# Kernel tuning notes

Measured on AMD Instinct MI355X. Metric: run time of the kernel, lower is better.

The kernel has to match this reference:

```python
import jax, jax.numpy as jnp
import numpy as np

M = 10000; D = 10000; FG = 256; FD = 256; K = 64
EX = 320000; EY = 320000


def setup_inputs() -> dict:
    key = jax.random.key(0)
    ks = jax.random.split(key, 32)
    s = 0.05  # weight scale
    inp = {}
    inp['x_m'] = jax.random.normal(ks[0], (M, FG), jnp.float32)
    inp['x_d'] = jax.random.normal(ks[1], (D, FD), jnp.float32)
    inp['edge_index_x'] = jax.random.randint(ks[2], (2, EX), 0, M)
    inp['edge_index_y'] = jax.random.randint(ks[3], (2, EY), 0, D)
    # GAT layer params (PyG layout: W [in, H*C], att [H, C], bias [H*C])
    inp['Wx1'] = jax.random.normal(ks[4], (FG, 2 * FG), jnp.float32) * s
    inp['ax1_src'] = jax.random.normal(ks[5], (2, FG), jnp.float32) * s
    inp['ax1_dst'] = jax.random.normal(ks[6], (2, FG), jnp.float32) * s
    inp['bx1'] = jnp.zeros((2 * FG,), jnp.float32)
    inp['Wx2'] = jax.random.normal(ks[7], (2 * FG, FG), jnp.float32) * s
    inp['ax2_src'] = jax.random.normal(ks[8], (1, FG), jnp.float32) * s
    inp['ax2_dst'] = jax.random.normal(ks[9], (1, FG), jnp.float32) * s
    inp['bx2'] = jnp.zeros((FG,), jnp.float32)
    inp['Wy1'] = jax.random.normal(ks[10], (FD, 2 * FD), jnp.float32) * s
    inp['ay1_src'] = jax.random.normal(ks[11], (2, FD), jnp.float32) * s
    inp['ay1_dst'] = jax.random.normal(ks[12], (2, FD), jnp.float32) * s
    inp['by1'] = jnp.zeros((2 * FD,), jnp.float32)
    inp['Wy2'] = jax.random.normal(ks[13], (2 * FD, FD), jnp.float32) * s
    inp['ay2_src'] = jax.random.normal(ks[14], (1, FD), jnp.float32) * s
    inp['ay2_dst'] = jax.random.normal(ks[15], (1, FD), jnp.float32) * s
    inp['by2'] = jnp.zeros((FD,), jnp.float32)
    # MLP heads
    inp['lwx1'] = jax.random.normal(ks[16], (FG, 256), jnp.float32) * s
    inp['lbx1'] = jnp.zeros((256,), jnp.float32)
    inp['lwx2'] = jax.random.normal(ks[17], (256, 128), jnp.float32) * s
    inp['lbx2'] = jnp.zeros((128,), jnp.float32)
    inp['lwx3'] = jax.random.normal(ks[18], (128, K), jnp.float32) * s
    inp['lbx3'] = jnp.zeros((K,), jnp.float32)
    inp['lwy1'] = jax.random.normal(ks[19], (FD, 256), jnp.float32) * s
    inp['lby1'] = jnp.zeros((256,), jnp.float32)
    inp['lwy2'] = jax.random.normal(ks[20], (256, 128), jnp.float32) * s
    inp['lby2'] = jnp.zeros((128,), jnp.float32)
    inp['lwy3'] = jax.random.normal(ks[21], (128, K), jnp.float32) * s
    inp['lby3'] = jnp.zeros((K,), jnp.float32)
    return inp


def gat_conv(x, src, dst, W, a_src, a_dst, b, n):
    # PyG GATConv, add_self_loops=False, negative_slope=0.2, concat=True
    H, C = a_src.shape
    xp = (x @ W).reshape(-1, H, C)                      # [N, H, C]
    al_s = jnp.einsum('nhc,hc->nh', xp, a_src)          # [N, H]
    al_d = jnp.einsum('nhc,hc->nh', xp, a_dst)
    e = jax.nn.leaky_relu(al_s[src] + al_d[dst], 0.2)   # [E, H]
    # softmax over edges grouped by destination node
    mx = jax.ops.segment_max(e, dst, num_segments=n)
    ee = jnp.exp(e - mx[dst])
    denom = jax.ops.segment_sum(ee, dst, num_segments=n)
    alpha = ee / (denom[dst] + 1e-16)                   # [E, H]
    out = jax.ops.segment_sum(xp[src] * alpha[:, :, None], dst, num_segments=n)
    return out.reshape(n, H * C) + b


def mlp3(h, w1, b1, w2, b2, w3, b3):
    h = jax.nn.relu(h @ w1 + b1)
    h = jax.nn.relu(h @ w2 + b2)
    return jax.nn.relu(h @ w3 + b3)


def reference(x_m, x_d, edge_index_x, edge_index_y,
              Wx1, ax1_src, ax1_dst, bx1, Wx2, ax2_src, ax2_dst, bx2,
              Wy1, ay1_src, ay1_dst, by1, Wy2, ay2_src, ay2_dst, by2,
              lwx1, lbx1, lwx2, lbx2, lwx3, lbx3,
              lwy1, lby1, lwy2, lby2, lwy3, lby3):
    sx, dx = edge_index_x[0], edge_index_x[1]
    sy, dy = edge_index_y[0], edge_index_y[1]
    X1 = jax.nn.relu(gat_conv(x_m, sx, dx, Wx1, ax1_src, ax1_dst, bx1, M))
    X = jax.nn.relu(gat_conv(X1, sx, dx, Wx2, ax2_src, ax2_dst, bx2, M))
    Y1 = jax.nn.relu(gat_conv(x_d, sy, dy, Wy1, ay1_src, ay1_dst, by1, D))
    Y = jax.nn.relu(gat_conv(Y1, sy, dy, Wy2, ay2_src, ay2_dst, by2, D))
    x = mlp3(X, lwx1, lbx1, lwx2, lbx2, lwx3, lbx3)     # [M, K]
    y = mlp3(Y, lwy1, lby1, lwy2, lby2, lwy3, lby3)     # [D, K]
    return x @ y.T                                      # [M, D]
```

## Files before the change

kernel.cpp:

```cpp
#include <hip/hip_runtime.h>
#include <cstddef>
#include <cstdint>

#define NODES 10000
#define EDGES 320000

typedef __attribute__((ext_vector_type(8))) short bf16x8;
typedef __attribute__((ext_vector_type(4))) float f32x4;

__device__ inline short bf16rn(float x){
    union { float f; unsigned u; } v; v.f = x;
    unsigned r = (v.u + 0x7FFFu + ((v.u >> 16) & 1u)) >> 16;
    return (short)r;
}
__device__ inline float bf16tof(short h){
    union { float f; unsigned u; } v; v.u = ((unsigned)(unsigned short)h) << 16;
    return v.f;
}

__global__ void count2_kernel(const int* __restrict__ ex, const int* __restrict__ ey,
                              int* __restrict__ counts){
    int e = blockIdx.x*256 + threadIdx.x;
    if (e < 2*EDGES){
        int d = (e < EDGES) ? ex[EDGES + e] : (ey[e] + NODES);
        atomicAdd(&counts[d], 1);
    }
}

__global__ __launch_bounds__(1024) void scan_kernel(const int* __restrict__ counts,
                                                    int* __restrict__ rowptr, int N){
    __shared__ int part[1024];
    int t = threadIdx.x;
    int chunk = (N + 1023) / 1024;
    int b0 = t * chunk;
    int s = 0;
    for (int i=0;i<chunk;i++){ int idx=b0+i; if (idx<N) s += counts[idx]; }
    part[t] = s;
    __syncthreads();
    for (int off=1; off<1024; off<<=1){
        int v = (t>=off) ? part[t-off] : 0;
        __syncthreads();
        part[t] += v;
        __syncthreads();
    }
    int excl = (t==0) ? 0 : part[t-1];
    for (int i=0;i<chunk;i++){
        int idx=b0+i;
        if (idx<N){ rowptr[idx]=excl; excl += counts[idx]; }
    }
    if (t==1023) rowptr[N] = part[1023];
}

__global__ void fill2_kernel(const int* __restrict__ ex, const int* __restrict__ ey,
                             int* __restrict__ cursor, int* __restrict__ col){
    int e = blockIdx.x*256 + threadIdx.x;
    if (e < 2*EDGES){
        int s, d;
        if (e < EDGES){ s = ex[e]; d = ex[EDGES+e]; }
        else          { s = ey[e-EDGES] + NODES; d = ey[e] + NODES; }
        int p = atomicAdd(&cursor[d], 1);
        col[p] = s;
    }
}

struct WtJob { const float* W; const float* a; float* out; int K; int H; int h; };
struct WtJobs { WtJob j[12]; };
__global__ __launch_bounds__(256) void wtilde_kernel(WtJobs js){
    WtJob jb = js.j[blockIdx.x];
    const int C = 256;
    for (int k = threadIdx.x; k < jb.K; k += 256){
        const float* wr = jb.W + (size_t)k*(jb.H*C) + jb.h*C;
        const float* ar = jb.a + jb.h*C;
        float s = 0.f;
        for (int c=0;c<C;c++) s += wr[c]*ar[c];
        jb.out[k*jb.H + jb.h] = s;
    }
}

struct StJob { const float* B; short* th; short* tl; int K; int N; };
struct StJobs { StJob j[10]; };
__global__ __launch_bounds__(256) void splitT_batch(StJobs js){
    StJob jb = js.j[blockIdx.z];
    int n0 = blockIdx.x*32, k0 = blockIdx.y*32;
    if (n0 >= jb.N || k0 >= jb.K) return;
    __shared__ float tile[32][33];
    int tx = threadIdx.x, ty = threadIdx.y;
    #pragma unroll
    for (int r=0;r<4;r++){ int k = ty + r*8; tile[k][tx] = jb.B[(size_t)(k0+k)*jb.N + n0 + tx]; }
    __syncthreads();
    #pragma unroll
    for (int r=0;r<4;r++){
        int n = ty + r*8;
        float v = tile[tx][n];
        short h = bf16rn(v);
        jb.th[(size_t)(n0+n)*jb.K + k0 + tx] = h;
        jb.tl[(size_t)(n0+n)*jb.K + k0 + tx] = bf16rn(v - bf16tof(h));
    }
}

__global__ void split_in_kernel(const float* __restrict__ x0, const float* __restrict__ x1,
                                short* __restrict__ h, short* __restrict__ l){
    int i = (blockIdx.x*256 + threadIdx.x)*4;
    const int HALF = NODES*256;
    if (i >= 2*HALF) return;
    const float* src = (i < HALF) ? (x0 + i) : (x1 + (i - HALF));
    float4 v = *(const float4*)src;
    short h0=bf16rn(v.x), h1=bf16rn(v.y), h2=bf16rn(v.z), h3=bf16rn(v.w);
    short4 hv; hv.x=h0; hv.y=h1; hv.z=h2; hv.w=h3;
    short4 lv; lv.x=bf16rn(v.x-bf16tof(h0)); lv.y=bf16rn(v.y-bf16tof(h1));
    lv.z=bf16rn(v.z-bf16tof(h2)); lv.w=bf16rn(v.w-bf16tof(h3));
    *(short4*)&h[i] = hv;
    *(short4*)&l[i] = lv;
}

struct GemmJob {
    const short* Ah; const short* Al; const short* Bh; const short* Bl;
    float* C; short* Ch; short* Cl; const float* bias;
};
__global__ __launch_bounds__(256) void gemm_ps(GemmJob j0, GemmJob j1,
        int Mr, int Nr, int Kr, int relu)
{
    GemmJob j = (blockIdx.z == 0) ? j0 : j1;
    __shared__ short Ash[96][88], Asl[96][88], Bsh[64][88], Bsl[64][88];
    int t = threadIdx.x;
    int lane = t & 63, wave = t >> 6;
    int wm = (wave >> 1) * 48, wn = (wave & 1) * 32;
    int m0 = blockIdx.y * 96, n0 = blockIdx.x * 64;

    f32x4 acc[3][2];
    #pragma unroll
    for (int i=0;i<3;i++)
      #pragma unroll
      for (int jj=0;jj<2;jj++)
        #pragma unroll
        for (int r=0;r<4;r++) acc[i][jj][r] = 0.f;

    int arow = t >> 3;
    int ablk = (t & 7) * 8;

    for (int k0 = 0; k0 < Kr; k0 += 64){
        #pragma unroll
        for (int rep=0; rep<3; rep++){
            int row = arow + rep*32;
            int gr = m0 + row; gr = gr < Mr ? gr : Mr-1;
            size_t off = (size_t)gr*Kr + k0 + ablk;
            *(int4*)&Ash[row][ablk] = *(const int4*)&j.Ah[off];
            *(int4*)&Asl[row][ablk] = *(const int4*)&j.Al[off];
        }
        #pragma unroll
        for (int rep=0; rep<2; rep++){
            int row = arow + rep*32;
            int gn = n0 + row; gn = gn < Nr ? gn : Nr-1;
            size_t off = (size_t)gn*Kr + k0 + ablk;
            *(int4*)&Bsh[row][ablk] = *(const int4*)&j.Bh[off];
            *(int4*)&Bsl[row][ablk] = *(const int4*)&j.Bl[off];
        }
        __syncthreads();
        #pragma unroll
        for (int ks=0; ks<2; ks++){
            int kk = ks*32 + (lane>>4)*8;
            bf16x8 bh[2], bl[2];
            #pragma unroll
            for (int jj=0;jj<2;jj++){
                bh[jj] = *(const bf16x8*)&Bsh[wn + jj*16 + (lane&15)][kk];
                bl[jj] = *(const bf16x8*)&Bsl[wn + jj*16 + (lane&15)][kk];
            }
            #pragma unroll
            for (int i=0;i<3;i++){
                bf16x8 ah = *(const bf16x8*)&Ash[wm + i*16 + (lane&15)][kk];
                bf16x8 al = *(const bf16x8*)&Asl[wm + i*16 + (lane&15)][kk];
                #pragma unroll
                for (int jj=0;jj<2;jj++){
                    acc[i][jj] = __builtin_amdgcn_mfma_f32_16x16x32_bf16(ah, bh[jj], acc[i][jj], 0,0,0);
                    acc[i][jj] = __builtin_amdgcn_mfma_f32_16x16x32_bf16(al, bh[jj], acc[i][jj], 0,0,0);
                    acc[i][jj] = __builtin_amdgcn_mfma_f32_16x16x32_bf16(ah, bl[jj], acc[i][jj], 0,0,0);
                }
            }
        }
        __syncthreads();
    }
    #pragma unroll
    for (int i=0;i<3;i++){
        int rbase = m0 + wm + i*16 + ((lane>>4)<<2);
        #pragma unroll
        for (int jj=0;jj<2;jj++){
            int colg = n0 + wn + jj*16 + (lane&15);
            if (colg >= Nr) continue;
            float bv = j.bias ? j.bias[colg] : 0.f;
            #pragma unroll
            for (int r=0;r<4;r++){
                int rg = rbase + r;
                if (rg < Mr){
                    float v = acc[i][jj][r] + bv;
                    if (relu) v = v > 0.f ? v : 0.f;
                    if (j.C) j.C[(size_t)rg*Nr + colg] = v;
                    if (j.Ch){
                        short hh = bf16rn(v);
                        j.Ch[(size_t)rg*Nr + colg] = hh;
                        j.Cl[(size_t)rg*Nr + colg] = bf16rn(v - bf16tof(hh));
                    }
                }
            }
        }
    }
}

template<int H>
__global__ __launch_bounds__(256) void algemv(const float* __restrict__ A0,
        const float* __restrict__ A1, const float* __restrict__ wtS,
        const float* __restrict__ wtD, int K,
        float* __restrict__ als, float* __restrict__ ald)
{
    int node = blockIdx.x*4 + (threadIdx.x>>6);
    int lane = threadIdx.x & 63;
    if (node >= 2*NODES) return;
    int g = node >= NODES;
    const float* A = g ? (A1 + (size_t)(node-NODES)*K) : (A0 + (size_t)node*K);
    const float* ws = wtS + (size_t)g*K*H;
    const float* wd = wtD + (size_t)g*K*H;
    float ss[H], sd[H];
    #pragma unroll
    for (int h=0;h<H;h++){ ss[h]=0.f; sd[h]=0.f; }
    for (int k=lane; k<K; k+=64){
        float v = A[k];
        #pragma unroll
        for (int h=0;h<H;h++){ ss[h] += v*ws[k*H+h]; sd[h] += v*wd[k*H+h]; }
    }
    #pragma unroll
    for (int off=32; off; off>>=1){
        #pragma unroll
        for (int h=0;h<H;h++){ ss[h] += __shfl_xor(ss[h], off); sd[h] += __shfl_xor(sd[h], off); }
    }
    if (lane==0){
        #pragma unroll
        for (int h=0;h<H;h++){ als[node*H+h]=ss[h]; ald[node*H+h]=sd[h]; }
    }
}

template<int H>
__global__ __launch_bounds__(256) void alpha_kernel(const int* __restrict__ rowptr,
        const int* __restrict__ col, const float* __restrict__ als,
        const float* __restrict__ ald, float* __restrict__ alpha)
{
    int node = blockIdx.x*4 + (threadIdx.x>>6);
    int lane = threadIdx.x & 63;
    if (node >= 2*NODES) return;
    int beg = rowptr[node], end = rowptr[node+1];
    #pragma unroll
    for (int h=0; h<H; h++){
        float ad = ald[node*H+h];
        float mx = -1e30f;
        for (int p=beg+lane; p<end; p+=64){
            float e = als[col[p]*H+h] + ad;
            e = e>0.f ? e : 0.2f*e;
            mx = fmaxf(mx, e);
        }
        #pragma unroll
        for (int off=32; off; off>>=1) mx = fmaxf(mx, __shfl_xor(mx, off));
        float sm = 0.f;
        for (int p=beg+lane; p<end; p+=64){
            float e = als[col[p]*H+h] + ad;
            e = e>0.f ? e : 0.2f*e;
            sm += __expf(e - mx);
        }
        #pragma unroll
        for (int off=32; off; off>>=1) sm += __shfl_xor(sm, off);
        float inv = 1.f/(sm + 1e-16f);
        for (int p=beg+lane; p<end; p+=64){
            float e = als[col[p]*H+h] + ad;
            e = e>0.f ? e : 0.2f*e;
            alpha[(size_t)p*H + h] = __expf(e - mx)*inv;
        }
    }
}

template<int W, int H>
__global__ __launch_bounds__(256) void agg_ps(const float* __restrict__ xp,
        const float* __restrict__ alpha, const int* __restrict__ rowptr,
        const int* __restrict__ col, const float* __restrict__ bias0,
        const float* __restrict__ bias1, float* __restrict__ out,
        short* __restrict__ outH, short* __restrict__ outL)
{
    int node = blockIdx.x*4 + (threadIdx.x>>6);
    int lane = threadIdx.x & 63;
    if (node >= 2*NODES) return;
    int beg = rowptr[node], end = rowptr[node+1];
    constexpr int NF = W/64;
    int lb = lane*NF;
    int hsel = (H==2) ? (lane>>5) : 0;
    float4 a0 = make_float4(0.f,0.f,0.f,0.f);
    float4 a1 = make_float4(0.f,0.f,0.f,0.f);
    for (int p=beg; p<end; p++){
        int s = col[p];
        float av = alpha[(size_t)p*H + hsel];
        const float* row = xp + (size_t)s*W + lb;
        float4 v0 = *(const float4*)row;
        a0.x += av*v0.x; a0.y += av*v0.y; a0.z += av*v0.z; a0.w += av*v0.w;
        if (NF==8){
            float4 v1 = *(const float4*)(row+4);
            a1.x += av*v1.x; a1.y += av*v1.y; a1.z += av*v1.z; a1.w += av*v1.w;
        }
    }
    const float* bs = (node >= NODES) ? bias1 : bias0;
    float4 bv = *(const float4*)&bs[lb];
    float r0 = fmaxf(a0.x+bv.x, 0.f), r1 = fmaxf(a0.y+bv.y, 0.f);
    float r2 = fmaxf(a0.z+bv.z, 0.f), r3 = fmaxf(a0.w+bv.w, 0.f);
    size_t base = (size_t)node*W + lb;
    if (out){ float4 o = make_float4(r0,r1,r2,r3); *(float4*)&out[base] = o; }
    short4 hh, ll;
    hh.x=bf16rn(r0); hh.y=bf16rn(r1); hh.z=bf16rn(r2); hh.w=bf16rn(r3);
    ll.x=bf16rn(r0-bf16tof(hh.x)); ll.y=bf16rn(r1-bf16tof(hh.y));
    ll.z=bf16rn(r2-bf16tof(hh.z)); ll.w=bf16rn(r3-bf16tof(hh.w));
    *(short4*)&outH[base] = hh;
    *(short4*)&outL[base] = ll;
    if (NF==8){
        float4 bw = *(const float4*)&bs[lb+4];
        float s0 = fmaxf(a1.x+bw.x, 0.f), s1 = fmaxf(a1.y+bw.y, 0.f);
        float s2 = fmaxf(a1.z+bw.z, 0.f), s3 = fmaxf(a1.w+bw.w, 0.f);
        if (out){ float4 o = make_float4(s0,s1,s2,s3); *(float4*)&out[base+4] = o; }
        hh.x=bf16rn(s0); hh.y=bf16rn(s1); hh.z=bf16rn(s2); hh.w=bf16rn(s3);
        ll.x=bf16rn(s0-bf16tof(hh.x)); ll.y=bf16rn(s1-bf16tof(hh.y));
        ll.z=bf16rn(s2-bf16tof(hh.z)); ll.w=bf16rn(s3-bf16tof(hh.w));
        *(short4*)&outH[base+4] = hh;
        *(short4*)&outL[base+4] = ll;
    }
}

extern "C" void kernel_launch(void* const* d_in, const int* in_sizes, int n_in,
                              void* d_out, int out_size, void* d_ws, size_t ws_size,
                              hipStream_t stream)
{
    const float* x_m  = (const float*)d_in[0];
    const float* x_d  = (const float*)d_in[1];
    const int*   eix  = (const int*)d_in[2];
    const int*   eiy  = (const int*)d_in[3];
    const float* Wx1  = (const float*)d_in[4];
    const float* ax1s = (const float*)d_in[5];
    const float* ax1d = (const float*)d_in[6];
    const float* bx1  = (const float*)d_in[7];
    const float* Wx2  = (const float*)d_in[8];
    const float* ax2s = (const float*)d_in[9];
    const float* ax2d = (const float*)d_in[10];
    const float* bx2  = (const float*)d_in[11];
    const float* Wy1  = (const float*)d_in[12];
    const float* ay1s = (const float*)d_in[13];
    const float* ay1d = (const float*)d_in[14];
    const float* by1  = (const float*)d_in[15];
    const float* Wy2  = (const float*)d_in[16];
    const float* ay2s = (const float*)d_in[17];
    const float* ay2d = (const float*)d_in[18];
    const float* by2  = (const float*)d_in[19];
    const float* lwx1 = (const float*)d_in[20];
    const float* lbx1 = (const float*)d_in[21];
    const float* lwx2 = (const float*)d_in[22];
    const float* lbx2 = (const float*)d_in[23];
    const float* lwx3 = (const float*)d_in[24];
    const float* lbx3 = (const float*)d_in[25];
    const float* lwy1 = (const float*)d_in[26];
    const float* lby1 = (const float*)d_in[27];
    const float* lwy2 = (const float*)d_in[28];
    const float* lby2 = (const float*)d_in[29];
    const float* lwy3 = (const float*)d_in[30];
    const float* lby3 = (const float*)d_in[31];

    const int N = NODES, E = EDGES, N2 = 2*NODES;
    char* ws = (char*)d_ws;
    size_t off = 0;
    auto alloc = [&](size_t bytes)->char*{
        size_t a = (off + 255) & ~(size_t)255;
        off = a + bytes;
        return ws + a;
    };
    int* rowptr = (int*)alloc((size_t)(N2+1)*4);
    int* cursor = (int*)alloc((size_t)N2*4);
    int* counts = (int*)alloc((size_t)N2*4);
    int* colidx = (int*)alloc((size_t)2*E*4);
    float* alphaA = (float*)alloc((size_t)2*E*2*4);
    short* xinh = (short*)alloc((size_t)N2*256*2);
    short* xinl = (short*)alloc((size_t)N2*256*2);
    float* xp   = (float*)alloc((size_t)N2*512*4);
    float* als1 = (float*)alloc((size_t)N2*2*4);
    float* ald1 = (float*)alloc((size_t)N2*2*4);
    float* bufA = (float*)alloc((size_t)N2*512*4);
    short* bufAh = (short*)alloc((size_t)N2*512*2);
    short* bufAl = (short*)alloc((size_t)N2*512*2);
    float* xp2  = (float*)alloc((size_t)N2*256*4);
    float* als2 = (float*)alloc((size_t)N2*4);
    float* ald2 = (float*)alloc((size_t)N2*4);
    short* bufBh = (short*)alloc((size_t)N2*256*2);
    short* bufBl = (short*)alloc((size_t)N2*256*2);
    short* m1h = (short*)alloc((size_t)N2*256*2);
    short* m1l = (short*)alloc((size_t)N2*256*2);
    short* m2h = (short*)alloc((size_t)N2*128*2);
    short* m2l = (short*)alloc((size_t)N2*128*2);
    short* m3h = (short*)alloc((size_t)N2*64*2);
    short* m3l = (short*)alloc((size_t)N2*64*2);
    float* wt1s = (float*)alloc((size_t)2*256*2*4);
    float* wt1d = (float*)alloc((size_t)2*256*2*4);
    float* wt2s = (float*)alloc((size_t)2*512*4);
    float* wt2d = (float*)alloc((size_t)2*512*4);
    auto sal = [&](size_t n)->short*{ return (short*)alloc(n*2); };
    short* w1h0 = sal(512*256), *w1l0 = sal(512*256), *w1h1 = sal(512*256), *w1l1 = sal(512*256);
    short* w2h0 = sal(256*512), *w2l0 = sal(256*512), *w2h1 = sal(256*512), *w2l1 = sal(256*512);
    short* l1h0 = sal(256*256), *l1l0 = sal(256*256), *l1h1 = sal(256*256), *l1l1 = sal(256*256);
    short* l2h0 = sal(128*256), *l2l0 = sal(128*256), *l2h1 = sal(128*256), *l2l1 = sal(128*256);
    short* l3h0 = sal(64*128),  *l3l0 = sal(64*128),  *l3h1 = sal(64*128),  *l3l1 = sal(64*128);

    hipMemsetAsync(counts, 0, (size_t)N2*4, stream);
    count2_kernel<<<(2*E+255)/256, 256, 0, stream>>>(eix, eiy, counts);
    scan_kernel<<<1, 1024, 0, stream>>>(counts, rowptr, N2);
    hipMemcpyAsync(cursor, rowptr, (size_t)N2*4, hipMemcpyDeviceToDevice, stream);
    fill2_kernel<<<(2*E+255)/256, 256, 0, stream>>>(eix, eiy, cursor, colidx);

    WtJobs wj;
    wj.j[0] = {Wx1, ax1s, wt1s,         256, 2, 0};
    wj.j[1] = {Wx1, ax1s, wt1s,         256, 2, 1};
    wj.j[2] = {Wx1, ax1d, wt1d,         256, 2, 0};
    wj.j[3] = {Wx1, ax1d, wt1d,         256, 2, 1};
    wj.j[4] = {Wy1, ay1s, wt1s+256*2,   256, 2, 0};
    wj.j[5] = {Wy1, ay1s, wt1s+256*2,   256, 2, 1};
    wj.j[6] = {Wy1, ay1d, wt1d+256*2,   256, 2, 0};
    wj.j[7] = {Wy1, ay1d, wt1d+256*2,   256, 2, 1};
    wj.j[8] = {Wx2, ax2s, wt2s,         512, 1, 0};
    wj.j[9] = {Wx2, ax2d, wt2d,         512, 1, 0};
    wj.j[10]= {Wy2, ay2s, wt2s+512,     512, 1, 0};
    wj.j[11]= {Wy2, ay2d, wt2d+512,     512, 1, 0};
    wtilde_kernel<<<12, 256, 0, stream>>>(wj);

    StJobs sj;
    sj.j[0] = {Wx1,  w1h0, w1l0, 256, 512};
    sj.j[1] = {Wy1,  w1h1, w1l1, 256, 512};
    sj.j[2] = {Wx2,  w2h0, w2l0, 512, 256};
    sj.j[3] = {Wy2,  w2h1, w2l1, 512, 256};
    sj.j[4] = {lwx1, l1h0, l1l0, 256, 256};
    sj.j[5] = {lwy1, l1h1, l1l1, 256, 256};
    sj.j[6] = {lwx2, l2h0, l2l0, 256, 128};
    sj.j[7] = {lwy2, l2h1, l2l1, 256, 128};
    sj.j[8] = {lwx3, l3h0, l3l0, 128, 64};
    sj.j[9] = {lwy3, l3h1, l3l1, 128, 64};
    splitT_batch<<<dim3(16,16,10), dim3(32,8), 0, stream>>>(sj);

    split_in_kernel<<<(N2*256/4 + 255)/256, 256, 0, stream>>>(x_m, x_d, xinh, xinl);

    GemmJob jz = {nullptr,nullptr,nullptr,nullptr,nullptr,nullptr,nullptr,nullptr};

    {
        GemmJob a = {xinh, xinl, w1h0, w1l0, xp, nullptr, nullptr, nullptr};
        GemmJob b = {xinh + (size_t)N*256, xinl + (size_t)N*256, w1h1, w1l1,
                     xp + (size_t)N*512, nullptr, nullptr, nullptr};
        gemm_ps<<<dim3(8, (N+95)/96, 2), 256, 0, stream>>>(a, b, N, 512, 256, 0);
    }
    algemv<2><<<(N2+3)/4, 256, 0, stream>>>(x_m, x_d, wt1s, wt1d, 256, als1, ald1);
    alpha_kernel<2><<<(N2+3)/4, 256, 0, stream>>>(rowptr, colidx, als1, ald1, alphaA);
    agg_ps<512,2><<<(N2+3)/4, 256, 0, stream>>>(xp, alphaA, rowptr, colidx,
                                                bx1, by1, bufA, bufAh, bufAl);
    {
        GemmJob a = {bufAh, bufAl, w2h0, w2l0, xp2, nullptr, nullptr, nullptr};
        GemmJob b = {bufAh + (size_t)N*512, bufAl + (size_t)N*512, w2h1, w2l1,
                     xp2 + (size_t)N*256, nullptr, nullptr, nullptr};
        gemm_ps<<<dim3(4, (N+95)/96, 2), 256, 0, stream>>>(a, b, N, 256, 512, 0);
    }
    algemv<1><<<(N2+3)/4, 256, 0, stream>>>(bufA, bufA + (size_t)N*512, wt2s, wt2d, 512, als2, ald2);
    alpha_kernel<1><<<(N2+3)/4, 256, 0, stream>>>(rowptr, colidx, als2, ald2, alphaA);
    agg_ps<256,1><<<(N2+3)/4, 256, 0, stream>>>(xp2, alphaA, rowptr, colidx,
                                                bx2, by2, nullptr, bufBh, bufBl);
    {
        GemmJob a = {bufBh, bufBl, l1h0, l1l0, nullptr, m1h, m1l, lbx1};
        GemmJob b = {bufBh + (size_t)N*256, bufBl + (size_t)N*256, l1h1, l1l1,
                     nullptr, m1h + (size_t)N*256, m1l + (size_t)N*256, lby1};
        gemm_ps<<<dim3(4, (N+95)/96, 2), 256, 0, stream>>>(a, b, N, 256, 256, 1);
    }
    {
        GemmJob a = {m1h, m1l, l2h0, l2l0, nullptr, m2h, m2l, lbx2};
        GemmJob b = {m1h + (size_t)N*256, m1l + (size_t)N*256, l2h1, l2l1,
                     nullptr, m2h + (size_t)N*128, m2l + (size_t)N*128, lby2};
        gemm_ps<<<dim3(2, (N+95)/96, 2), 256, 0, stream>>>(a, b, N, 128, 256, 1);
    }
    {
        GemmJob a = {m2h, m2l, l3h0, l3l0, nullptr, m3h, m3l, lbx3};
        GemmJob b = {m2h + (size_t)N*128, m2l + (size_t)N*128, l3h1, l3l1,
                     nullptr, m3h + (size_t)N*64, m3l + (size_t)N*64, lby3};
        gemm_ps<<<dim3(1, (N+95)/96, 2), 256, 0, stream>>>(a, b, N, 64, 128, 1);
    }
    {
        GemmJob a = {m3h, m3l, m3h + (size_t)N*64, m3l + (size_t)N*64,
                     (float*)d_out, nullptr, nullptr, nullptr};
        gemm_ps<<<dim3((N+63)/64, (N+95)/96, 1), 256, 0, stream>>>(a, jz, N, N, 64, 0);
    }
}
```

Before: 1.148 ms.

## Fuse GAT attention logits and softmax into aggregation, stage GEMM epilogue via LDS

Folds the layer-1 attention logit GEMV into the input split kernel and computes the layer-2 logits inside the layer-1 aggregation using atomic adds. Softmax normalisation moves into the aggregation kernel, and each wave now handles a 256-column half. This removes the separate alpha kernel, the alpha buffer and the fp32 bufA round trip. The GEMM epilogue now goes through shared memory so global stores are vectorised float4/short4 writes. The trade-off is recomputing the softmax max and sum once per half-wave, plus atomics and extra memsets.

New measurement: 1.047 ms. 1.1x faster.

```diff
diff --git a/kernel.cpp b/kernel.cpp
--- a/kernel.cpp
+++ b/kernel.cpp
@@ -98,19 +98,43 @@
     }
 }
 
-__global__ void split_in_kernel(const float* __restrict__ x0, const float* __restrict__ x1,
-                                short* __restrict__ h, short* __restrict__ l){
-    int i = (blockIdx.x*256 + threadIdx.x)*4;
-    const int HALF = NODES*256;
-    if (i >= 2*HALF) return;
-    const float* src = (i < HALF) ? (x0 + i) : (x1 + (i - HALF));
-    float4 v = *(const float4*)src;
-    short h0=bf16rn(v.x), h1=bf16rn(v.y), h2=bf16rn(v.z), h3=bf16rn(v.w);
-    short4 hv; hv.x=h0; hv.y=h1; hv.z=h2; hv.w=h3;
-    short4 lv; lv.x=bf16rn(v.x-bf16tof(h0)); lv.y=bf16rn(v.y-bf16tof(h1));
-    lv.z=bf16rn(v.z-bf16tof(h2)); lv.w=bf16rn(v.w-bf16tof(h3));
-    *(short4*)&h[i] = hv;
-    *(short4*)&l[i] = lv;
+__global__ __launch_bounds__(256) void split_in2(const float* __restrict__ x0,
+        const float* __restrict__ x1, const float* __restrict__ wt1s,
+        const float* __restrict__ wt1d, short* __restrict__ hh, short* __restrict__ ll,
+        float* __restrict__ als, float* __restrict__ ald)
+{
+    int node = blockIdx.x*4 + (threadIdx.x>>6);
+    int lane = threadIdx.x & 63;
+    if (node >= 2*NODES) return;
+    int g = node >= NODES;
+    const float* X = g ? (x1 + (size_t)(node-NODES)*256) : (x0 + (size_t)node*256);
+    const float* ws = wt1s + g*512;
+    const float* wd = wt1d + g*512;
+    float4 v = *(const float4*)&X[lane*4];
+    short4 hv, lv;
+    hv.x=bf16rn(v.x); hv.y=bf16rn(v.y); hv.z=bf16rn(v.z); hv.w=bf16rn(v.w);
+    lv.x=bf16rn(v.x-bf16tof(hv.x)); lv.y=bf16rn(v.y-bf16tof(hv.y));
+    lv.z=bf16rn(v.z-bf16tof(hv.z)); lv.w=bf16rn(v.w-bf16tof(hv.w));
+    size_t base = (size_t)node*256 + lane*4;
+    *(short4*)&hh[base] = hv;
+    *(short4*)&ll[base] = lv;
+    float s0=0.f,s1=0.f,d0=0.f,d1=0.f;
+    float vv[4] = {v.x,v.y,v.z,v.w};
+    #pragma unroll
+    for (int q=0;q<4;q++){
+        int k = lane*4+q;
+        s0 += vv[q]*ws[k*2+0]; s1 += vv[q]*ws[k*2+1];
+        d0 += vv[q]*wd[k*2+0]; d1 += vv[q]*wd[k*2+1];
+    }
+    #pragma unroll
+    for (int off=32; off; off>>=1){
+        s0 += __shfl_xor(s0,off); s1 += __shfl_xor(s1,off);
+        d0 += __shfl_xor(d0,off); d1 += __shfl_xor(d1,off);
+    }
+    if (lane==0){
+        als[node*2]=s0; als[node*2+1]=s1;
+        ald[node*2]=d0; ald[node*2+1]=d1;
+    }
 }
 
 struct GemmJob {
@@ -121,7 +145,11 @@
         int Mr, int Nr, int Kr, int relu)
 {
     GemmJob j = (blockIdx.z == 0) ? j0 : j1;
-    __shared__ short Ash[96][88], Asl[96][88], Bsh[64][88], Bsl[64][88];
+    __shared__ short smem[28160];
+    short (*Ash)[88] = (short(*)[88])(smem);
+    short (*Asl)[88] = (short(*)[88])(smem + 8448);
+    short (*Bsh)[88] = (short(*)[88])(smem + 16896);
+    short (*Bsl)[88] = (short(*)[88])(smem + 22528);
     int t = threadIdx.x;
     int lane = t & 63, wave = t >> 6;
     int wm = (wave >> 1) * 48, wn = (wave & 1) * 32;
@@ -179,150 +207,118 @@
         }
         __syncthreads();
     }
+    float* eplds = (float*)smem;
+    const int EL = 68;
     #pragma unroll
     for (int i=0;i<3;i++){
-        int rbase = m0 + wm + i*16 + ((lane>>4)<<2);
+        int row = wm + i*16 + ((lane>>4)<<2);
         #pragma unroll
         for (int jj=0;jj<2;jj++){
-            int colg = n0 + wn + jj*16 + (lane&15);
-            if (colg >= Nr) continue;
-            float bv = j.bias ? j.bias[colg] : 0.f;
+            int colL = wn + jj*16 + (lane&15);
             #pragma unroll
-            for (int r=0;r<4;r++){
-                int rg = rbase + r;
-                if (rg < Mr){
-                    float v = acc[i][jj][r] + bv;
-                    if (relu) v = v > 0.f ? v : 0.f;
-                    if (j.C) j.C[(size_t)rg*Nr + colg] = v;
-                    if (j.Ch){
-                        short hh = bf16rn(v);
-                        j.Ch[(size_t)rg*Nr + colg] = hh;
-                        j.Cl[(size_t)rg*Nr + colg] = bf16rn(v - bf16tof(hh));
-                    }
-                }
-            }
-        }
-    }
-}
-
-template<int H>
-__global__ __launch_bounds__(256) void algemv(const float* __restrict__ A0,
-        const float* __restrict__ A1, const float* __restrict__ wtS,
-        const float* __restrict__ wtD, int K,
-        float* __restrict__ als, float* __restrict__ ald)
+            for (int r=0;r<4;r++)
+                eplds[(row+r)*EL + colL] = acc[i][jj][r];
+        }
+    }
+    __syncthreads();
+    int tx = t & 15, ty = t >> 4;
+    int colg = n0 + tx*4;
+    float4 bv = make_float4(0.f,0.f,0.f,0.f);
+    if (j.bias && colg < Nr) bv = *(const float4*)&j.bias[colg];
+    #pragma unroll
+    for (int rep=0; rep<6; rep++){
+        int row = ty + rep*16;
+        int rg = m0 + row;
+        if (rg >= Mr || colg >= Nr) continue;
+        float4 v = *(float4*)&eplds[row*EL + tx*4];
+        v.x += bv.x; v.y += bv.y; v.z += bv.z; v.w += bv.w;
+        if (relu){
+            v.x = fmaxf(v.x,0.f); v.y = fmaxf(v.y,0.f);
+            v.z = fmaxf(v.z,0.f); v.w = fmaxf(v.w,0.f);
+        }
+        if (j.C) *(float4*)&j.C[(size_t)rg*Nr + colg] = v;
+        if (j.Ch){
+            short4 hv, lv;
+            hv.x=bf16rn(v.x); hv.y=bf16rn(v.y); hv.z=bf16rn(v.z); hv.w=bf16rn(v.w);
+            lv.x=bf16rn(v.x-bf16tof(hv.x)); lv.y=bf16rn(v.y-bf16tof(hv.y));
+            lv.z=bf16rn(v.z-bf16tof(hv.z)); lv.w=bf16rn(v.w-bf16tof(hv.w));
+            *(short4*)&j.Ch[(size_t)rg*Nr + colg] = hv;
+            *(short4*)&j.Cl[(size_t)rg*Nr + colg] = lv;
+        }
+    }
+}
+
+template<int W, int H, int DOT>
+__global__ __launch_bounds__(256) void agg_fused(const float* __restrict__ xp,
+        const float* __restrict__ als, const float* __restrict__ ald,
+        const int* __restrict__ rowptr, const int* __restrict__ col,
+        const float* __restrict__ bias0, const float* __restrict__ bias1,
+        short* __restrict__ outH, short* __restrict__ outL,
+        const float* __restrict__ w2s, const float* __restrict__ w2d,
+        float* __restrict__ als2, float* __restrict__ ald2)
 {
-    int node = blockIdx.x*4 + (threadIdx.x>>6);
+    constexpr int HALVES = W/256;
+    int w = blockIdx.x*4 + (threadIdx.x>>6);
     int lane = threadIdx.x & 63;
+    int node = w / HALVES;
+    int half = w - node*HALVES;
     if (node >= 2*NODES) return;
-    int g = node >= NODES;
-    const float* A = g ? (A1 + (size_t)(node-NODES)*K) : (A0 + (size_t)node*K);
-    const float* ws = wtS + (size_t)g*K*H;
-    const float* wd = wtD + (size_t)g*K*H;
-    float ss[H], sd[H];
-    #pragma unroll
-    for (int h=0;h<H;h++){ ss[h]=0.f; sd[h]=0.f; }
-    for (int k=lane; k<K; k+=64){
-        float v = A[k];
-        #pragma unroll
-        for (int h=0;h<H;h++){ ss[h] += v*ws[k*H+h]; sd[h] += v*wd[k*H+h]; }
-    }
-    #pragma unroll
-    for (int off=32; off; off>>=1){
-        #pragma unroll
-        for (int h=0;h<H;h++){ ss[h] += __shfl_xor(ss[h], off); sd[h] += __shfl_xor(sd[h], off); }
-    }
-    if (lane==0){
-        #pragma unroll
-        for (int h=0;h<H;h++){ als[node*H+h]=ss[h]; ald[node*H+h]=sd[h]; }
-    }
-}
-
-template<int H>
-__global__ __launch_bounds__(256) void alpha_kernel(const int* __restrict__ rowptr,
-        const int* __restrict__ col, const float* __restrict__ als,
-        const float* __restrict__ ald, float* __restrict__ alpha)
-{
-    int node = blockIdx.x*4 + (threadIdx.x>>6);
-    int lane = threadIdx.x & 63;
-    if (node >= 2*NODES) return;
+    int h = (H==2) ? half : 0;
     int beg = rowptr[node], end = rowptr[node+1];
-    #pragma unroll
-    for (int h=0; h<H; h++){
-        float ad = ald[node*H+h];
-        float mx = -1e30f;
-        for (int p=beg+lane; p<end; p+=64){
-            float e = als[col[p]*H+h] + ad;
-            e = e>0.f ? e : 0.2f*e;
-            mx = fmaxf(mx, e);
-        }
-        #pragma unroll
-        for (int off=32; off; off>>=1) mx = fmaxf(mx, __shfl_xor(mx, off));
-        float sm = 0.f;
-        for (int p=beg+lane; p<end; p+=64){
-            float e = als[col[p]*H+h] + ad;
-            e = e>0.f ? e : 0.2f*e;
-            sm += __expf(e - mx);
-        }
-        #pragma unroll
-        for (int off=32; off; off>>=1) sm += __shfl_xor(sm, off);
-        float inv = 1.f/(sm + 1e-16f);
-        for (int p=beg+lane; p<end; p+=64){
-            float e = als[col[p]*H+h] + ad;
-            e = e>0.f ? e : 0.2f*e;
-            alpha[(size_t)p*H + h] = __expf(e - mx)*inv;
-        }
-    }
-}
-
-template<int W, int H>
-__global__ __launch_bounds__(256) void agg_ps(const float* __restrict__ xp,
-        const float* __restrict__ alpha, const int* __restrict__ rowptr,
-        const int* __restrict__ col, const float* __restrict__ bias0,
-        const float* __restrict__ bias1, float* __restrict__ out,
-        short* __restrict__ outH, short* __restrict__ outL)
-{
-    int node = blockIdx.x*4 + (threadIdx.x>>6);
-    int lane = threadIdx.x & 63;
-    if (node >= 2*NODES) return;
-    int beg = rowptr[node], end = rowptr[node+1];
-    constexpr int NF = W/64;
-    int lb = lane*NF;
-    int hsel = (H==2) ? (lane>>5) : 0;
-    float4 a0 = make_float4(0.f,0.f,0.f,0.f);
-    float4 a1 = make_float4(0.f,0.f,0.f,0.f);
+    float ad = ald[node*H+h];
+    float mx = -1e30f;
+    for (int p=beg+lane; p<end; p+=64){
+        float e = als[col[p]*H+h] + ad;
+        e = e>0.f ? e : 0.2f*e;
+        mx = fmaxf(mx, e);
+    }
+    #pragma unroll
+    for (int off=32; off; off>>=1) mx = fmaxf(mx, __shfl_xor(mx, off));
+    float sm = 0.f;
+    for (int p=beg+lane; p<end; p+=64){
+        float e = als[col[p]*H+h] + ad;
+        e = e>0.f ? e : 0.2f*e;
+        sm += __expf(e - mx);
+    }
+    #pragma unroll
+    for (int off=32; off; off>>=1) sm += __shfl_xor(sm, off);
+    float inv = 1.f/(sm + 1e-16f);
+
+    int cbase = half*256 + lane*4;
+    float4 a = make_float4(0.f,0.f,0.f,0.f);
     for (int p=beg; p<end; p++){
         int s = col[p];
-        float av = alpha[(size_t)p*H + hsel];
-        const float* row = xp + (size_t)s*W + lb;
-        float4 v0 = *(const float4*)row;
-        a0.x += av*v0.x; a0.y += av*v0.y; a0.z += av*v0.z; a0.w += av*v0.w;
-        if (NF==8){
-            float4 v1 = *(const float4*)(row+4);
-            a1.x += av*v1.x; a1.y += av*v1.y; a1.z += av*v1.z; a1.w += av*v1.w;
-        }
+        float e = als[s*H+h] + ad;
+        e = e>0.f ? e : 0.2f*e;
+        float wv = __expf(e - mx)*inv;
+        float4 v = *(const float4*)&xp[(size_t)s*W + cbase];
+        a.x += wv*v.x; a.y += wv*v.y; a.z += wv*v.z; a.w += wv*v.w;
     }
     const float* bs = (node >= NODES) ? bias1 : bias0;
-    float4 bv = *(const float4*)&bs[lb];
-    float r0 = fmaxf(a0.x+bv.x, 0.f), r1 = fmaxf(a0.y+bv.y, 0.f);
-    float r2 = fmaxf(a0.z+bv.z, 0.f), r3 = fmaxf(a0.w+bv.w, 0.f);
-    size_t base = (size_t)node*W + lb;
-    if (out){ float4 o = make_float4(r0,r1,r2,r3); *(float4*)&out[base] = o; }
-    short4 hh, ll;
-    hh.x=bf16rn(r0); hh.y=bf16rn(r1); hh.z=bf16rn(r2); hh.w=bf16rn(r3);
-    ll.x=bf16rn(r0-bf16tof(hh.x)); ll.y=bf16rn(r1-bf16tof(hh.y));
-    ll.z=bf16rn(r2-bf16tof(hh.z)); ll.w=bf16rn(r3-bf16tof(hh.w));
-    *(short4*)&outH[base] = hh;
-    *(short4*)&outL[base] = ll;
-    if (NF==8){
-        float4 bw = *(const float4*)&bs[lb+4];
-        float s0 = fmaxf(a1.x+bw.x, 0.f), s1 = fmaxf(a1.y+bw.y, 0.f);
-        float s2 = fmaxf(a1.z+bw.z, 0.f), s3 = fmaxf(a1.w+bw.w, 0.f);
-        if (out){ float4 o = make_float4(s0,s1,s2,s3); *(float4*)&out[base+4] = o; }
-        hh.x=bf16rn(s0); hh.y=bf16rn(s1); hh.z=bf16rn(s2); hh.w=bf16rn(s3);
-        ll.x=bf16rn(s0-bf16tof(hh.x)); ll.y=bf16rn(s1-bf16tof(hh.y));
-        ll.z=bf16rn(s2-bf16tof(hh.z)); ll.w=bf16rn(s3-bf16tof(hh.w));
-        *(short4*)&outH[base+4] = hh;
-        *(short4*)&outL[base+4] = ll;
+    float4 bv = *(const float4*)&bs[cbase];
+    float r0 = fmaxf(a.x+bv.x, 0.f), r1 = fmaxf(a.y+bv.y, 0.f);
+    float r2 = fmaxf(a.z+bv.z, 0.f), r3 = fmaxf(a.w+bv.w, 0.f);
+    size_t base = (size_t)node*W + cbase;
+    short4 hv, lv;
+    hv.x=bf16rn(r0); hv.y=bf16rn(r1); hv.z=bf16rn(r2); hv.w=bf16rn(r3);
+    lv.x=bf16rn(r0-bf16tof(hv.x)); lv.y=bf16rn(r1-bf16tof(hv.y));
+    lv.z=bf16rn(r2-bf16tof(hv.z)); lv.w=bf16rn(r3-bf16tof(hv.w));
+    *(short4*)&outH[base] = hv;
+    *(short4*)&outL[base] = lv;
+    if (DOT){
+        int g = node >= NODES;
+        const float* s2 = w2s + (size_t)g*W;
+        const float* d2 = w2d + (size_t)g*W;
+        float ss = r0*s2[cbase] + r1*s2[cbase+1] + r2*s2[cbase+2] + r3*s2[cbase+3];
+        float dd = r0*d2[cbase] + r1*d2[cbase+1] + r2*d2[cbase+2] + r3*d2[cbase+3];
+        #pragma unroll
+        for (int off=32; off; off>>=1){
+            ss += __shfl_xor(ss, off); dd += __shfl_xor(dd, off);
+        }
+        if (lane==0){
+            atomicAdd(&als2[node], ss);
+            atomicAdd(&ald2[node], dd);
+        }
     }
 }
 
@@ -375,13 +371,11 @@
     int* cursor = (int*)alloc((size_t)N2*4);
     int* counts = (int*)alloc((size_t)N2*4);
     int* colidx = (int*)alloc((size_t)2*E*4);
-    float* alphaA = (float*)alloc((size_t)2*E*2*4);
     short* xinh = (short*)alloc((size_t)N2*256*2);
     short* xinl = (short*)alloc((size_t)N2*256*2);
     float* xp   = (float*)alloc((size_t)N2*512*4);
     float* als1 = (float*)alloc((size_t)N2*2*4);
     float* ald1 = (float*)alloc((size_t)N2*2*4);
-    float* bufA = (float*)alloc((size_t)N2*512*4);
     short* bufAh = (short*)alloc((size_t)N2*512*2);
     short* bufAl = (short*)alloc((size_t)N2*512*2);
     float* xp2  = (float*)alloc((size_t)N2*256*4);
@@ -407,6 +401,9 @@
     short* l3h0 = sal(64*128),  *l3l0 = sal(64*128),  *l3h1 = sal(64*128),  *l3l1 = sal(64*128);
 
     hipMemsetAsync(counts, 0, (size_t)N2*4, stream);
+    hipMemsetAsync(als2, 0, (size_t)N2*4, stream);
+    hipMemsetAsync(ald2, 0, (size_t)N2*4, stream);
+
     count2_kernel<<<(2*E+255)/256, 256, 0, stream>>>(eix, eiy, counts);
     scan_kernel<<<1, 1024, 0, stream>>>(counts, rowptr, N2);
     hipMemcpyAsync(cursor, rowptr, (size_t)N2*4, hipMemcpyDeviceToDevice, stream);
@@ -440,7 +437,7 @@
     sj.j[9] = {lwy3, l3h1, l3l1, 128, 64};
     splitT_batch<<<dim3(16,16,10), dim3(32,8), 0, stream>>>(sj);
 
-    split_in_kernel<<<(N2*256/4 + 255)/256, 256, 0, stream>>>(x_m, x_d, xinh, xinl);
+    split_in2<<<(N2+3)/4, 256, 0, stream>>>(x_m, x_d, wt1s, wt1d, xinh, xinl, als1, ald1);
 
     GemmJob jz = {nullptr,nullptr,nullptr,nullptr,nullptr,nullptr,nullptr,nullptr};
 
@@ -450,20 +447,16 @@
                      xp + (size_t)N*512, nullptr, nullptr, nullptr};
         gemm_ps<<<dim3(8, (N+95)/96, 2), 256, 0, stream>>>(a, b, N, 512, 256, 0);
     }
-    algemv<2><<<(N2+3)/4, 256, 0, stream>>>(x_m, x_d, wt1s, wt1d, 256, als1, ald1);
-    alpha_kernel<2><<<(N2+3)/4, 256, 0, stream>>>(rowptr, colidx, als1, ald1, alphaA);
-    agg_ps<512,2><<<(N2+3)/4, 256, 0, stream>>>(xp, alphaA, rowptr, colidx,
-                                                bx1, by1, bufA, bufAh, bufAl);
+    agg_fused<512,2,1><<<(N2*2+3)/4, 256, 0, stream>>>(xp, als1, ald1, rowptr, colidx,
+            bx1, by1, bufAh, bufAl, wt2s, wt2d, als2, ald2);
     {
         GemmJob a = {bufAh, bufAl, w2h0, w2l0, xp2, nullptr, nullptr, nullptr};
         GemmJob b = {bufAh + (size_t)N*512, bufAl + (size_t)N*512, w2h1, w2l1,
                      xp2 + (size_t)N*256, nullptr, nullptr, nullptr};
         gemm_ps<<<dim3(4, (N+95)/96, 2), 256, 0, stream>>>(a, b, N, 256, 512, 0);
     }
-    algemv<1><<<(N2+3)/4, 256, 0, stream>>>(bufA, bufA + (size_t)N*512, wt2s, wt2d, 512, als2, ald2);
-    alpha_kernel<1><<<(N2+3)/4, 256, 0, stream>>>(rowptr, colidx, als2, ald2, alphaA);
-    agg_ps<256,1><<<(N2+3)/4, 256, 0, stream>>>(xp2, alphaA, rowptr, colidx,
-                                                bx2, by2, nullptr, bufBh, bufBl);
+    agg_fused<256,1,0><<<(N2+3)/4, 256, 0, stream>>>(xp2, als2, ald2, rowptr, colidx,
+            bx2, by2, bufBh, bufBl, nullptr, nullptr, nullptr, nullptr);
     {
         GemmJob a = {bufBh, bufBl, l1h0, l1l0, nullptr, m1h, m1l, lbx1};
         GemmJob b = {bufBh + (size_t)N*256, bufBl + (size_t)N*256, l1h1, l1l1,
```
